# Performance work log

Hardware: AMD Instinct MI355X
Metric: run time of the kernel (lower is better)

## Reference

```python
import jax, jax.numpy as jnp
import numpy as np

N = 2048      # n_nodes
D = 512       # n_channels
AVG_DEG = 16  # average graph degree


def setup_inputs() -> dict:
    key = jax.random.key(0)
    k1, k2, k3 = jax.random.split(key, 3)
    # node features [N, D]
    x = jax.random.normal(k1, (N, D), dtype=jnp.float32)
    # random symmetric graph -> combinatorial Laplacian L = D - A
    E = N * AVG_DEG
    src = jax.random.randint(k2, (E,), 0, N)
    dst = jax.random.randint(k3, (E,), 0, N)
    A = jnp.zeros((N, N), jnp.float32).at[src, dst].add(1.0)
    A = (A + A.T) * 0.5
    A = A * (1.0 - jnp.eye(N, dtype=jnp.float32))  # drop self loops
    deg = A.sum(axis=1)
    L = jnp.diag(deg) - A
    # learned diffusion time (scalar parameter, ic=0.5)
    t = jnp.float32(0.5)
    return {"x": x, "L": L, "t": t}


def reference(x, L, t):
    # forward clamps diffusion_time to >= 1e-8
    tt = jnp.maximum(t, jnp.float32(1e-8))
    # heat kernel: expm(-t * L); the original loops over channels applying
    # compute_diffusion(x[:, [i]], t, L, 'matrix_exp') == expm(-t L) @ x[:, i],
    # which is exactly one dense matmul fused across all channels.
    P = jax.scipy.linalg.expm(-tt * L)  # [N, N]
    return P @ x  # [N, D]
```

## Files before the change

kernel.cpp:

```cpp
#include <hip/hip_runtime.h>

#define N_NODES 2048
#define N_CH    512
#define K_CHEB  48
#define NNZ_MAX 131072
#define NB      256

#define OFF_DIAG   0
#define OFF_SCAL   8192
#define OFF_PERM   12288
#define OFF_BASE   20480
#define OFF_CNTO   28672
#define OFF_GCNT   36864
#define OFF_PKV    40960

__device__ __forceinline__ float b2f(unsigned short u) {
    return __uint_as_float(((unsigned int)u) << 16);
}
__device__ __forceinline__ bool detect32(const unsigned int* tw) {
    return (tw[0] & 0xFFFFu) == 0u;
}
__device__ __forceinline__ unsigned short encE(int col, float v) {
    unsigned int n = (unsigned int)(-2.0f * v + 0.5f);
    return (unsigned short)(((unsigned int)col << 5) | (n & 31u));
}

__global__ void __launch_bounds__(256)
k_prep(const void* __restrict__ Lp, const unsigned int* __restrict__ tw,
       float* __restrict__ diagv, int* __restrict__ basev, int* __restrict__ cnto,
       int* __restrict__ gcnt, unsigned short* __restrict__ pkv) {
    __shared__ unsigned short stage[4][N_NODES];
    __shared__ int scnt[4];
    __shared__ int sbase;
    int w    = threadIdx.x >> 6;
    int lane = threadIdx.x & 63;
    int row  = blockIdx.x * 4 + w;
    bool is32 = detect32(tw);
    int run = 0; float dv = 0.f;
    if (is32) {
        const float4* rf4 = (const float4*)((const float*)Lp + (size_t)row * N_NODES);
        #pragma unroll
        for (int i = 0; i < 8; i++) {
            int j = i * 64 + lane;
            float4 v = rf4[j];
            if (j == (row >> 2)) {
                int rm = row & 3;
                if      (rm == 0) { dv = v.x; v.x = 0.f; }
                else if (rm == 1) { dv = v.y; v.y = 0.f; }
                else if (rm == 2) { dv = v.z; v.z = 0.f; }
                else              { dv = v.w; v.w = 0.f; }
            }
            int c0 = j * 4;
            int lc = (v.x != 0.f) + (v.y != 0.f) + (v.z != 0.f) + (v.w != 0.f);
            int xs = lc;
            #pragma unroll
            for (int d = 1; d < 64; d <<= 1) { int n = __shfl_up(xs, d); if (lane >= d) xs += n; }
            int o = run + xs - lc;
            if (v.x != 0.f) stage[w][o++] = encE(c0 + 0, v.x);
            if (v.y != 0.f) stage[w][o++] = encE(c0 + 1, v.y);
            if (v.z != 0.f) stage[w][o++] = encE(c0 + 2, v.z);
            if (v.w != 0.f) stage[w][o++] = encE(c0 + 3, v.w);
            run += __shfl(xs, 63);
        }
    } else {
        const unsigned short* rp = (const unsigned short*)Lp + (size_t)row * N_NODES;
        for (int c0 = 0; c0 < N_NODES; c0 += 64) {
            float v = b2f(rp[c0 + lane]);
            if (c0 + lane == row) { dv = v; v = 0.f; }
            bool p = (v != 0.f);
            unsigned long long m = __ballot(p);
            int off = __popcll(m & ((1ull << lane) - 1ull));
            if (p) stage[w][run + off] = encE(c0 + lane, v);
            run += (int)__popcll(m);
        }
    }
    #pragma unroll
    for (int o = 32; o; o >>= 1) dv += __shfl_xor(dv, o);
    int padded = (run + 7) & ~7;
    for (int e = run + lane; e < padded; e += 64) stage[w][e] = 0;
    if (lane == 0) scnt[w] = padded;
    __syncthreads();
    if (threadIdx.x == 0)
        sbase = atomicAdd(gcnt, scnt[0] + scnt[1] + scnt[2] + scnt[3]);
    __syncthreads();
    int myb = sbase;
    for (int w2 = 0; w2 < w; w2++) myb += scnt[w2];
    if (lane == 0) { basev[row] = myb; cnto[row] = padded >> 3; diagv[row] = dv; }
    const unsigned int* s32 = (const unsigned int*)stage[w];
    unsigned int* p32 = (unsigned int*)pkv + (myb >> 1);
    for (int i = lane; i < (padded >> 1); i += 64) p32[i] = s32[i];
}

__global__ void k_scan(const float* __restrict__ diagv, float* __restrict__ scal,
                       const void* __restrict__ tp, const int* __restrict__ cnto,
                       int* __restrict__ perm) {
    __shared__ float  fmaxs[256];
    __shared__ double dz[1];
    __shared__ float  cabs[K_CHEB + 1];
    __shared__ int    hist[256];
    __shared__ int    hstart[256];
    int t = threadIdx.x;
    hist[t] = 0;
    float mx = 0.f;
    #pragma unroll
    for (int i = 0; i < 8; i++) mx = fmaxf(mx, diagv[t * 8 + i]);
    fmaxs[t] = mx;
    __syncthreads();
    for (int o = 128; o; o >>= 1) {
        if (t < o) fmaxs[t] = fmaxf(fmaxs[t], fmaxs[t + o]);
        __syncthreads();
    }
    if (t == 0) {
        bool is32 = detect32((const unsigned int*)tp);
        float tt = is32 ? ((const float*)tp)[0] : b2f(((const unsigned short*)tp)[0]);
        tt = fmaxf(tt, 1e-8f);
        float beta = 2.0f * fmaxs[0];
        scal[0] = (beta > 0.f) ? 2.0f / beta : 0.f;
        dz[0] = (beta > 0.f) ? (double)tt * (double)beta * 0.5 : 0.0;
    }
    __syncthreads();
    if (t <= K_CHEB) {
        int k = t;
        double z = dz[0];
        double emz = exp(-z), h = 0.5 * z, h2 = h * h;
        double term = 1.0;
        for (int j = 1; j <= k; j++) term *= h / (double)j;
        double sum = term;
        for (int m = 1; m < 300; m++) {
            term *= h2 / ((double)m * (double)(m + k));
            sum += term;
            if (term == 0.0 || term < sum * 1e-18) break;
        }
        double ck = emz * sum * (k == 0 ? 1.0 : 2.0);
        if (k & 1) ck = -ck;
        scal[16 + k] = (float)ck;
        cabs[k] = (float)fabs(ck);
    }
    __syncthreads();
    if (t == 0) {
        int keff = 1;
        for (int k = K_CHEB; k >= 2; k--)
            if (cabs[k] >= 2.5e-4f) { keff = k; break; }
        scal[1] = (float)keff;
    }
    #pragma unroll
    for (int i = 0; i < 8; i++) {
        int q = min(cnto[t * 8 + i], 255);
        atomicAdd(&hist[q], 1);
    }
    __syncthreads();
    if (t == 0) {
        int acc = 0;
        for (int l = 255; l >= 0; l--) { hstart[l] = acc; acc += hist[l]; }
    }
    __syncthreads();
    #pragma unroll
    for (int i = 0; i < 8; i++) {
        int idx = t * 8 + i;
        int q = min(cnto[idx], 255);
        int pos = atomicAdd(&hstart[q], 1);
        perm[pos] = idx;
    }
}

__device__ __forceinline__ void oct_fma(const float2* __restrict__ cur, uint4 q,
                                        float& ax, float& ay, float& bx, float& by) {
    #pragma unroll
    for (int i = 0; i < 4; i++) {
        unsigned int u = (i == 0) ? q.x : (i == 1) ? q.y : (i == 2) ? q.z : q.w;
        unsigned int e0 = u & 0xFFFFu, e1 = u >> 16;
        float2 c0 = cur[e0 >> 5];
        float2 c1 = cur[e1 >> 5];
        float n0 = (float)(e0 & 31u), n1 = (float)(e1 & 31u);
        ax += n0 * c0.x; ay += n0 * c0.y;
        bx += n1 * c1.x; by += n1 * c1.y;
    }
}

__device__ __forceinline__ float2 gatherO(const float2* __restrict__ cur,
                                          const uint4* __restrict__ s4,
                                          int j0, int j1) {
    float ax = 0.f, ay = 0.f, bx = 0.f, by = 0.f;
    int j = j0;
    if (j + 2 <= j1) {
        uint4 q0 = s4[j], q1 = s4[j + 1];
        j += 2;
        while (j + 2 <= j1) {
            uint4 p0 = s4[j], p1 = s4[j + 1];
            oct_fma(cur, q0, ax, ay, bx, by);
            oct_fma(cur, q1, ax, ay, bx, by);
            q0 = p0; q1 = p1;
            j += 2;
        }
        oct_fma(cur, q0, ax, ay, bx, by);
        oct_fma(cur, q1, ax, ay, bx, by);
    }
    if (j < j1) oct_fma(cur, s4[j], ax, ay, bx, by);
    return make_float2(ax + bx, ay + by);
}

__global__ void __launch_bounds__(1024, 4)
k_cheb(const void* __restrict__ x, const unsigned int* __restrict__ tw,
       const int* __restrict__ basev, const int* __restrict__ cnto,
       const float* __restrict__ diagv, const unsigned short* __restrict__ pkv,
       const float* __restrict__ scal, const int* __restrict__ perm,
       void* __restrict__ out) {
    __shared__ float2 bufA[N_NODES];
    __shared__ float2 bufB[N_NODES];
    __shared__ float  scoef[K_CHEB + 1];
    int t  = threadIdx.x;
    int cb = blockIdx.x * 2;
    bool is32 = detect32(tw);
    if (t <= K_CHEB) scoef[t] = scal[16 + t];
    int ra = perm[t], rb = perm[2047 - t];
    int na = cnto[ra], nb = cnto[rb];
    int pa0 = basev[ra] >> 3, pb0 = basev[rb] >> 3;
    const uint4* s4 = (const uint4*)pkv;
    float da = diagv[ra], db = diagv[rb];
    float g = scal[0];
    int   K = (int)scal[1];

    float2 xa, xb;
    if (is32) {
        xa = *(const float2*)((const float*)x + (size_t)ra * N_CH + cb);
        xb = *(const float2*)((const float*)x + (size_t)rb * N_CH + cb);
    } else {
        const unsigned short* xp = (const unsigned short*)x;
        unsigned int wa = *(const unsigned int*)(xp + (size_t)ra * N_CH + cb);
        unsigned int wb = *(const unsigned int*)(xp + (size_t)rb * N_CH + cb);
        xa = make_float2(b2f((unsigned short)(wa & 0xFFFFu)), b2f((unsigned short)(wa >> 16)));
        xb = make_float2(b2f((unsigned short)(wb & 0xFFFFu)), b2f((unsigned short)(wb >> 16)));
    }
    bufA[ra] = xa; bufA[rb] = xb;
    __syncthreads();

    float gm = -0.5f * g;
    float ia = g * da - 1.f, ib = g * db - 1.f;
    float2 aa = gatherO(bufA, s4, pa0, pa0 + na);
    float2 ab = gatherO(bufA, s4, pb0, pb0 + nb);
    float2 pva = xa, pvb = xb;
    float2 cua = make_float2(gm * aa.x + ia * xa.x, gm * aa.y + ia * xa.y);
    float2 cub = make_float2(gm * ab.x + ib * xb.x, gm * ab.y + ib * xb.y);
    float c0 = scoef[0], c1 = scoef[1];
    float2 oa = make_float2(c0 * xa.x + c1 * cua.x, c0 * xa.y + c1 * cua.y);
    float2 ob = make_float2(c0 * xb.x + c1 * cub.x, c0 * xb.y + c1 * cub.y);
    bufB[ra] = cua; bufB[rb] = cub;
    __syncthreads();

    float gn  = -g;
    float dga = 2.f * g * da - 2.f, dgb = 2.f * g * db - 2.f;
    for (int k = 2; k <= K; k++) {
        const float2* rd = (k & 1) ? bufA : bufB;
        float2*       wr = (k & 1) ? bufB : bufA;
        float ck = scoef[k];
        float2 ba = gatherO(rd, s4, pa0, pa0 + na);
        float2 bb = gatherO(rd, s4, pb0, pb0 + nb);
        float2 tna = make_float2(gn * ba.x + dga * cua.x - pva.x,
                                 gn * ba.y + dga * cua.y - pva.y);
        float2 tnb = make_float2(gn * bb.x + dgb * cub.x - pvb.x,
                                 gn * bb.y + dgb * cub.y - pvb.y);
        pva = cua; cua = tna;
        pvb = cub; cub = tnb;
        oa.x += ck * tna.x; oa.y += ck * tna.y;
        ob.x += ck * tnb.x; ob.y += ck * tnb.y;
        wr[ra] = tna; wr[rb] = tnb;
        __syncthreads();
    }

    if (is32) {
        *(float2*)((float*)out + (size_t)ra * N_CH + cb) = oa;
        *(float2*)((float*)out + (size_t)rb * N_CH + cb) = ob;
    } else {
        unsigned int ua, ub;
        { unsigned int u0 = __float_as_uint(oa.x), u1 = __float_as_uint(oa.y);
          u0 = (u0 + 0x7FFFu + ((u0 >> 16) & 1u)) >> 16;
          u1 = (u1 + 0x7FFFu + ((u1 >> 16) & 1u)) >> 16;
          ua = u0 | (u1 << 16); }
        { unsigned int u0 = __float_as_uint(ob.x), u1 = __float_as_uint(ob.y);
          u0 = (u0 + 0x7FFFu + ((u0 >> 16) & 1u)) >> 16;
          u1 = (u1 + 0x7FFFu + ((u1 >> 16) & 1u)) >> 16;
          ub = u0 | (u1 << 16); }
        *(unsigned int*)((unsigned short*)out + (size_t)ra * N_CH + cb) = ua;
        *(unsigned int*)((unsigned short*)out + (size_t)rb * N_CH + cb) = ub;
    }
}

extern "C" void kernel_launch(void* const* d_in, const int* in_sizes, int n_in,
                              void* d_out, int out_size, void* d_ws, size_t ws_size,
                              hipStream_t stream) {
    const void* x  = d_in[0];
    const void* L  = d_in[1];
    const void* tp = d_in[2];
    const unsigned int* tw = (const unsigned int*)tp;

    char* ws = (char*)d_ws;
    float*          diagv = (float*)          (ws + OFF_DIAG);
    float*          scal  = (float*)          (ws + OFF_SCAL);
    int*            perm  = (int*)            (ws + OFF_PERM);
    int*            basev = (int*)            (ws + OFF_BASE);
    int*            cnto  = (int*)            (ws + OFF_CNTO);
    int*            gcnt  = (int*)            (ws + OFF_GCNT);
    unsigned short* pkv   = (unsigned short*) (ws + OFF_PKV);

    hipMemsetAsync(gcnt, 0, 4, stream);
    k_prep<<<512, 256, 0, stream>>>(L, tw, diagv, basev, cnto, gcnt, pkv);
    k_scan<<<1,   256, 0, stream>>>(diagv, scal, tp, cnto, perm);
    k_cheb<<<NB, 1024, 0, stream>>>(x, tw, basev, cnto, diagv, pkv, scal, perm, d_out);
}
```

Measured before the change: 177.4 us.

## Use fixed-capacity sparse rows and bank-rotate entries to cut LDS conflicts

Each row's packed sparse entries now sit in a fixed 128-slot region instead of a space handed out by a global atomic. This removes the memset, the atomic offset allocation and the base-offset array. A new k_bank kernel reorders each row's entries by column bank group, rotated by the row's thread slot, so lanes of a wavefront gather from the shared-memory vector on different LDS banks at the same step. In exchange there is an extra kernel launch, and rows with more than 128 nonzeros would be truncated, which is only enforced on the bf16 path.

```diff
diff --git a/kernel.cpp b/kernel.cpp
--- a/kernel.cpp
+++ b/kernel.cpp
@@ -3,16 +3,16 @@
 #define N_NODES 2048
 #define N_CH    512
 #define K_CHEB  48
-#define NNZ_MAX 131072
+#define ROW_CAP 128
 #define NB      256
 
 #define OFF_DIAG   0
 #define OFF_SCAL   8192
 #define OFF_PERM   12288
-#define OFF_BASE   20480
+#define OFF_ROT    20480
 #define OFF_CNTO   28672
-#define OFF_GCNT   36864
 #define OFF_PKV    40960
+#define OFF_PKV2   (40960 + 524288)
 
 __device__ __forceinline__ float b2f(unsigned short u) {
     return __uint_as_float(((unsigned int)u) << 16);
@@ -27,11 +27,9 @@
 
 __global__ void __launch_bounds__(256)
 k_prep(const void* __restrict__ Lp, const unsigned int* __restrict__ tw,
-       float* __restrict__ diagv, int* __restrict__ basev, int* __restrict__ cnto,
-       int* __restrict__ gcnt, unsigned short* __restrict__ pkv) {
+       float* __restrict__ diagv, int* __restrict__ cnto,
+       unsigned short* __restrict__ pkv) {
     __shared__ unsigned short stage[4][N_NODES];
-    __shared__ int scnt[4];
-    __shared__ int sbase;
     int w    = threadIdx.x >> 6;
     int lane = threadIdx.x & 63;
     int row  = blockIdx.x * 4 + w;
@@ -70,30 +68,24 @@
             bool p = (v != 0.f);
             unsigned long long m = __ballot(p);
             int off = __popcll(m & ((1ull << lane) - 1ull));
-            if (p) stage[w][run + off] = encE(c0 + lane, v);
+            if (p && run + off < ROW_CAP) stage[w][run + off] = encE(c0 + lane, v);
             run += (int)__popcll(m);
         }
     }
     #pragma unroll
     for (int o = 32; o; o >>= 1) dv += __shfl_xor(dv, o);
+    run = min(run, ROW_CAP);
     int padded = (run + 7) & ~7;
     for (int e = run + lane; e < padded; e += 64) stage[w][e] = 0;
-    if (lane == 0) scnt[w] = padded;
-    __syncthreads();
-    if (threadIdx.x == 0)
-        sbase = atomicAdd(gcnt, scnt[0] + scnt[1] + scnt[2] + scnt[3]);
-    __syncthreads();
-    int myb = sbase;
-    for (int w2 = 0; w2 < w; w2++) myb += scnt[w2];
-    if (lane == 0) { basev[row] = myb; cnto[row] = padded >> 3; diagv[row] = dv; }
+    if (lane == 0) { cnto[row] = padded >> 3; diagv[row] = dv; }
     const unsigned int* s32 = (const unsigned int*)stage[w];
-    unsigned int* p32 = (unsigned int*)pkv + (myb >> 1);
+    unsigned int* p32 = (unsigned int*)pkv + row * (ROW_CAP / 2);
     for (int i = lane; i < (padded >> 1); i += 64) p32[i] = s32[i];
 }
 
 __global__ void k_scan(const float* __restrict__ diagv, float* __restrict__ scal,
                        const void* __restrict__ tp, const int* __restrict__ cnto,
-                       int* __restrict__ perm) {
+                       int* __restrict__ perm, int* __restrict__ rot16) {
     __shared__ float  fmaxs[256];
     __shared__ double dz[1];
     __shared__ float  cabs[K_CHEB + 1];
@@ -160,6 +152,35 @@
         int q = min(cnto[idx], 255);
         int pos = atomicAdd(&hstart[q], 1);
         perm[pos] = idx;
+        int thr = (pos < 1024) ? pos : (2047 - pos);
+        rot16[idx] = thr & 15;
+    }
+}
+
+__global__ void __launch_bounds__(256)
+k_bank(const unsigned short* __restrict__ pkv, const int* __restrict__ cnto,
+       const int* __restrict__ rot16, unsigned short* __restrict__ pkv2) {
+    int wid  = (blockIdx.x * blockDim.x + threadIdx.x) >> 6;
+    int lane = threadIdx.x & 63;
+    if (wid >= N_NODES) return;
+    int n   = cnto[wid] * 8;
+    int rot = rot16[wid];
+    const unsigned short* src = pkv  + wid * ROW_CAP;
+    unsigned short*       dst = pkv2 + wid * ROW_CAP;
+    bool v0 = lane < n, v1 = lane + 64 < n;
+    unsigned short e0 = v0 ? src[lane]      : 0;
+    unsigned short e1 = v1 ? src[lane + 64] : 0;
+    int k0 = ((int)((e0 >> 5) & 15) - rot) & 15;
+    int k1 = ((int)((e1 >> 5) & 15) - rot) & 15;
+    int pos = 0;
+    #pragma unroll
+    for (int b = 0; b < 16; b++) {
+        unsigned long long m0 = __ballot(v0 && k0 == b);
+        unsigned long long m1 = __ballot(v1 && k1 == b);
+        int c0 = __popcll(m0);
+        if (v0 && k0 == b) dst[pos +      __popcll(m0 & ((1ull << lane) - 1ull))] = e0;
+        if (v1 && k1 == b) dst[pos + c0 + __popcll(m1 & ((1ull << lane) - 1ull))] = e1;
+        pos += c0 + __popcll(m1);
     }
 }
 
@@ -201,10 +222,9 @@
 
 __global__ void __launch_bounds__(1024, 4)
 k_cheb(const void* __restrict__ x, const unsigned int* __restrict__ tw,
-       const int* __restrict__ basev, const int* __restrict__ cnto,
-       const float* __restrict__ diagv, const unsigned short* __restrict__ pkv,
-       const float* __restrict__ scal, const int* __restrict__ perm,
-       void* __restrict__ out) {
+       const int* __restrict__ cnto, const float* __restrict__ diagv,
+       const unsigned short* __restrict__ pkv2, const float* __restrict__ scal,
+       const int* __restrict__ perm, void* __restrict__ out) {
     __shared__ float2 bufA[N_NODES];
     __shared__ float2 bufB[N_NODES];
     __shared__ float  scoef[K_CHEB + 1];
@@ -214,8 +234,8 @@
     if (t <= K_CHEB) scoef[t] = scal[16 + t];
     int ra = perm[t], rb = perm[2047 - t];
     int na = cnto[ra], nb = cnto[rb];
-    int pa0 = basev[ra] >> 3, pb0 = basev[rb] >> 3;
-    const uint4* s4 = (const uint4*)pkv;
+    int pa0 = ra * (ROW_CAP / 8), pb0 = rb * (ROW_CAP / 8);
+    const uint4* s4 = (const uint4*)pkv2;
     float da = diagv[ra], db = diagv[rb];
     float g = scal[0];
     int   K = (int)scal[1];
@@ -297,13 +317,13 @@
     float*          diagv = (float*)          (ws + OFF_DIAG);
     float*          scal  = (float*)          (ws + OFF_SCAL);
     int*            perm  = (int*)            (ws + OFF_PERM);
-    int*            basev = (int*)            (ws + OFF_BASE);
+    int*            rot16 = (int*)            (ws + OFF_ROT);
     int*            cnto  = (int*)            (ws + OFF_CNTO);
-    int*            gcnt  = (int*)            (ws + OFF_GCNT);
     unsigned short* pkv   = (unsigned short*) (ws + OFF_PKV);
-
-    hipMemsetAsync(gcnt, 0, 4, stream);
-    k_prep<<<512, 256, 0, stream>>>(L, tw, diagv, basev, cnto, gcnt, pkv);
-    k_scan<<<1,   256, 0, stream>>>(diagv, scal, tp, cnto, perm);
-    k_cheb<<<NB, 1024, 0, stream>>>(x, tw, basev, cnto, diagv, pkv, scal, perm, d_out);
-}
+    unsigned short* pkv2  = (unsigned short*) (ws + OFF_PKV2);
+
+    k_prep<<<512, 256, 0, stream>>>(L, tw, diagv, cnto, pkv);
+    k_scan<<<1,   256, 0, stream>>>(diagv, scal, tp, cnto, perm, rot16);
+    k_bank<<<512, 256, 0, stream>>>(pkv, cnto, rot16, pkv2);
+    k_cheb<<<NB, 1024, 0, stream>>>(x, tw, cnto, diagv, pkv2, scal, perm, d_out);
+}
```

Measured after the change: 178.6 us. About the same (+0.7%).

## Tighten spectral bound with edge-based estimate and raise Chebyshev truncation threshold

Applied to the files above, without the earlier changes.

Adds a kernel that computes a tighter upper bound on the Laplacian's largest eigenvalue as the max over edges of d_i + d_j, replacing the 2*max-degree bound. A smaller spectral interval lowers z and so the number of Chebyshev terms needed. The coefficient cutoff for choosing the effective degree is also raised, which truncates the series earlier. Both cut the number of sparse matvec iterations, at the cost of an extra kernel launch and a looser accuracy margin.

```diff
diff --git a/kernel.cpp b/kernel.cpp
--- a/kernel.cpp
+++ b/kernel.cpp
@@ -91,30 +91,39 @@
     for (int i = lane; i < (padded >> 1); i += 64) p32[i] = s32[i];
 }
 
-__global__ void k_scan(const float* __restrict__ diagv, float* __restrict__ scal,
-                       const void* __restrict__ tp, const int* __restrict__ cnto,
+__global__ void __launch_bounds__(256)
+k_edge(const float* __restrict__ diagv, const int* __restrict__ basev,
+       const int* __restrict__ cnto, const unsigned short* __restrict__ pkv,
+       int* __restrict__ betam) {
+    int wid  = (blockIdx.x * blockDim.x + threadIdx.x) >> 6;
+    int lane = threadIdx.x & 63;
+    if (wid >= N_NODES) return;
+    float dr = diagv[wid];
+    int b = basev[wid], ne = cnto[wid] * 8;
+    float mx = 0.f;
+    for (int e = lane; e < ne; e += 64) {
+        unsigned short u = pkv[b + e];
+        if (u & 31u) mx = fmaxf(mx, dr + diagv[u >> 5]);
+    }
+    #pragma unroll
+    for (int o = 32; o; o >>= 1) mx = fmaxf(mx, __shfl_xor(mx, o));
+    if (lane == 0) atomicMax(betam, __float_as_int(mx));
+}
+
+__global__ void k_scan(float* __restrict__ scal, const void* __restrict__ tp,
+                       const int* __restrict__ cnto, const int* __restrict__ betam,
                        int* __restrict__ perm) {
-    __shared__ float  fmaxs[256];
     __shared__ double dz[1];
     __shared__ float  cabs[K_CHEB + 1];
     __shared__ int    hist[256];
     __shared__ int    hstart[256];
     int t = threadIdx.x;
     hist[t] = 0;
-    float mx = 0.f;
-    #pragma unroll
-    for (int i = 0; i < 8; i++) mx = fmaxf(mx, diagv[t * 8 + i]);
-    fmaxs[t] = mx;
-    __syncthreads();
-    for (int o = 128; o; o >>= 1) {
-        if (t < o) fmaxs[t] = fmaxf(fmaxs[t], fmaxs[t + o]);
-        __syncthreads();
-    }
     if (t == 0) {
         bool is32 = detect32((const unsigned int*)tp);
         float tt = is32 ? ((const float*)tp)[0] : b2f(((const unsigned short*)tp)[0]);
         tt = fmaxf(tt, 1e-8f);
-        float beta = 2.0f * fmaxs[0];
+        float beta = __int_as_float(betam[0]);
         scal[0] = (beta > 0.f) ? 2.0f / beta : 0.f;
         dz[0] = (beta > 0.f) ? (double)tt * (double)beta * 0.5 : 0.0;
     }
@@ -140,7 +149,7 @@
     if (t == 0) {
         int keff = 1;
         for (int k = K_CHEB; k >= 2; k--)
-            if (cabs[k] >= 2.5e-4f) { keff = k; break; }
+            if (cabs[k] >= 4e-4f) { keff = k; break; }
         scal[1] = (float)keff;
     }
     #pragma unroll
@@ -302,8 +311,9 @@
     int*            gcnt  = (int*)            (ws + OFF_GCNT);
     unsigned short* pkv   = (unsigned short*) (ws + OFF_PKV);
 
-    hipMemsetAsync(gcnt, 0, 4, stream);
+    hipMemsetAsync(gcnt, 0, 8, stream);
     k_prep<<<512, 256, 0, stream>>>(L, tw, diagv, basev, cnto, gcnt, pkv);
-    k_scan<<<1,   256, 0, stream>>>(diagv, scal, tp, cnto, perm);
+    k_edge<<<512, 256, 0, stream>>>(diagv, basev, cnto, pkv, gcnt + 1);
+    k_scan<<<1,   256, 0, stream>>>(scal, tp, cnto, gcnt + 1, perm);
     k_cheb<<<NB, 1024, 0, stream>>>(x, tw, basev, cnto, diagv, pkv, scal, perm, d_out);
 }
```

Measured after the change: 196.9 us. 11.0% more time.

## Fold scan kernel into Chebyshev kernel and use fixed-capacity per-row sparse storage

Applied to the files above, without the earlier changes.

Removes the memset and the single-block k_scan launch. Each k_cheb block now redundantly computes the spectral bound, the Chebyshev coefficients, the row permutation histogram and the effective degree in shared memory. Rows are stored at a fixed 96-entry capacity, which drops the global atomic offset allocation, but any row with more nonzeros is silently truncated. The spectral bound becomes the maximum of d_i + d_j over edges, which is tighter than 2*max(d), and the coefficient cutoff is loosened from 2.5e-4 to 4e-4, so fewer Chebyshev terms may run at some cost in accuracy.

```diff
diff --git a/kernel.cpp b/kernel.cpp
--- a/kernel.cpp
+++ b/kernel.cpp
@@ -3,16 +3,13 @@
 #define N_NODES 2048
 #define N_CH    512
 #define K_CHEB  48
-#define NNZ_MAX 131072
+#define ROW_CAP 96
+#define ROW_OCT (ROW_CAP / 8)
 #define NB      256
 
 #define OFF_DIAG   0
-#define OFF_SCAL   8192
-#define OFF_PERM   12288
-#define OFF_BASE   20480
-#define OFF_CNTO   28672
-#define OFF_GCNT   36864
-#define OFF_PKV    40960
+#define OFF_CNTO   8192
+#define OFF_PKV    16384
 
 __device__ __forceinline__ float b2f(unsigned short u) {
     return __uint_as_float(((unsigned int)u) << 16);
@@ -27,11 +24,9 @@
 
 __global__ void __launch_bounds__(256)
 k_prep(const void* __restrict__ Lp, const unsigned int* __restrict__ tw,
-       float* __restrict__ diagv, int* __restrict__ basev, int* __restrict__ cnto,
-       int* __restrict__ gcnt, unsigned short* __restrict__ pkv) {
+       float* __restrict__ diagv, int* __restrict__ cnto,
+       unsigned short* __restrict__ pkv) {
     __shared__ unsigned short stage[4][N_NODES];
-    __shared__ int scnt[4];
-    __shared__ int sbase;
     int w    = threadIdx.x >> 6;
     int lane = threadIdx.x & 63;
     int row  = blockIdx.x * 4 + w;
@@ -76,91 +71,13 @@
     }
     #pragma unroll
     for (int o = 32; o; o >>= 1) dv += __shfl_xor(dv, o);
+    run = min(run, ROW_CAP);
     int padded = (run + 7) & ~7;
     for (int e = run + lane; e < padded; e += 64) stage[w][e] = 0;
-    if (lane == 0) scnt[w] = padded;
-    __syncthreads();
-    if (threadIdx.x == 0)
-        sbase = atomicAdd(gcnt, scnt[0] + scnt[1] + scnt[2] + scnt[3]);
-    __syncthreads();
-    int myb = sbase;
-    for (int w2 = 0; w2 < w; w2++) myb += scnt[w2];
-    if (lane == 0) { basev[row] = myb; cnto[row] = padded >> 3; diagv[row] = dv; }
+    if (lane == 0) { cnto[row] = padded >> 3; diagv[row] = dv; }
     const unsigned int* s32 = (const unsigned int*)stage[w];
-    unsigned int* p32 = (unsigned int*)pkv + (myb >> 1);
+    unsigned int* p32 = (unsigned int*)pkv + row * (ROW_CAP / 2);
     for (int i = lane; i < (padded >> 1); i += 64) p32[i] = s32[i];
-}
-
-__global__ void k_scan(const float* __restrict__ diagv, float* __restrict__ scal,
-                       const void* __restrict__ tp, const int* __restrict__ cnto,
-                       int* __restrict__ perm) {
-    __shared__ float  fmaxs[256];
-    __shared__ double dz[1];
-    __shared__ float  cabs[K_CHEB + 1];
-    __shared__ int    hist[256];
-    __shared__ int    hstart[256];
-    int t = threadIdx.x;
-    hist[t] = 0;
-    float mx = 0.f;
-    #pragma unroll
-    for (int i = 0; i < 8; i++) mx = fmaxf(mx, diagv[t * 8 + i]);
-    fmaxs[t] = mx;
-    __syncthreads();
-    for (int o = 128; o; o >>= 1) {
-        if (t < o) fmaxs[t] = fmaxf(fmaxs[t], fmaxs[t + o]);
-        __syncthreads();
-    }
-    if (t == 0) {
-        bool is32 = detect32((const unsigned int*)tp);
-        float tt = is32 ? ((const float*)tp)[0] : b2f(((const unsigned short*)tp)[0]);
-        tt = fmaxf(tt, 1e-8f);
-        float beta = 2.0f * fmaxs[0];
-        scal[0] = (beta > 0.f) ? 2.0f / beta : 0.f;
-        dz[0] = (beta > 0.f) ? (double)tt * (double)beta * 0.5 : 0.0;
-    }
-    __syncthreads();
-    if (t <= K_CHEB) {
-        int k = t;
-        double z = dz[0];
-        double emz = exp(-z), h = 0.5 * z, h2 = h * h;
-        double term = 1.0;
-        for (int j = 1; j <= k; j++) term *= h / (double)j;
-        double sum = term;
-        for (int m = 1; m < 300; m++) {
-            term *= h2 / ((double)m * (double)(m + k));
-            sum += term;
-            if (term == 0.0 || term < sum * 1e-18) break;
-        }
-        double ck = emz * sum * (k == 0 ? 1.0 : 2.0);
-        if (k & 1) ck = -ck;
-        scal[16 + k] = (float)ck;
-        cabs[k] = (float)fabs(ck);
-    }
-    __syncthreads();
-    if (t == 0) {
-        int keff = 1;
-        for (int k = K_CHEB; k >= 2; k--)
-            if (cabs[k] >= 2.5e-4f) { keff = k; break; }
-        scal[1] = (float)keff;
-    }
-    #pragma unroll
-    for (int i = 0; i < 8; i++) {
-        int q = min(cnto[t * 8 + i], 255);
-        atomicAdd(&hist[q], 1);
-    }
-    __syncthreads();
-    if (t == 0) {
-        int acc = 0;
-        for (int l = 255; l >= 0; l--) { hstart[l] = acc; acc += hist[l]; }
-    }
-    __syncthreads();
-    #pragma unroll
-    for (int i = 0; i < 8; i++) {
-        int idx = t * 8 + i;
-        int q = min(cnto[idx], 255);
-        int pos = atomicAdd(&hstart[q], 1);
-        perm[pos] = idx;
-    }
 }
 
 __device__ __forceinline__ void oct_fma(const float2* __restrict__ cur, uint4 q,
@@ -201,24 +118,110 @@
 
 __global__ void __launch_bounds__(1024, 4)
 k_cheb(const void* __restrict__ x, const unsigned int* __restrict__ tw,
-       const int* __restrict__ basev, const int* __restrict__ cnto,
-       const float* __restrict__ diagv, const unsigned short* __restrict__ pkv,
-       const float* __restrict__ scal, const int* __restrict__ perm,
-       void* __restrict__ out) {
-    __shared__ float2 bufA[N_NODES];
-    __shared__ float2 bufB[N_NODES];
+       const int* __restrict__ cnto, const float* __restrict__ diagv,
+       const unsigned short* __restrict__ pkv, void* __restrict__ out) {
+    __shared__ float  bufA2[N_NODES * 2];
+    __shared__ float  bufB2[N_NODES * 2];
+    __shared__ float  sdiag[N_NODES];
+    __shared__ int    sperm[N_NODES];
+    __shared__ int    scnt[N_NODES];
     __shared__ float  scoef[K_CHEB + 1];
+    __shared__ float  cabs[K_CHEB + 1];
+    __shared__ int    hist[256];
+    __shared__ int    ibeta;
+    __shared__ double dzs;
+    __shared__ int    skeff;
+    float2* bufA = (float2*)bufA2;
+    float2* bufB = (float2*)bufB2;
+
     int t  = threadIdx.x;
     int cb = blockIdx.x * 2;
     bool is32 = detect32(tw);
-    if (t <= K_CHEB) scoef[t] = scal[16 + t];
-    int ra = perm[t], rb = perm[2047 - t];
-    int na = cnto[ra], nb = cnto[rb];
-    int pa0 = basev[ra] >> 3, pb0 = basev[rb] >> 3;
+    int r0 = t, r1 = t + 1024;
+
+    sdiag[r0] = diagv[r0]; sdiag[r1] = diagv[r1];
+    int q0 = cnto[r0], q1 = cnto[r1];
+    scnt[r0] = q0; scnt[r1] = q1;
+    if (t < 256) hist[t] = 0;
+    if (t == 0) ibeta = 0;
+    __syncthreads();
+    {
+        const uint4* s4 = (const uint4*)pkv;
+        float mx = 0.f;
+        #pragma unroll
+        for (int rr = 0; rr < 2; rr++) {
+            int r  = rr ? r1 : r0;
+            int no = rr ? q1 : q0;
+            float dr = sdiag[r];
+            for (int j = 0; j < no; j++) {
+                uint4 q = s4[r * ROW_OCT + j];
+                #pragma unroll
+                for (int i = 0; i < 4; i++) {
+                    unsigned int u = (i == 0) ? q.x : (i == 1) ? q.y : (i == 2) ? q.z : q.w;
+                    unsigned int e0 = u & 0xFFFFu, e1 = u >> 16;
+                    if (e0 & 31u) mx = fmaxf(mx, dr + sdiag[e0 >> 5]);
+                    if (e1 & 31u) mx = fmaxf(mx, dr + sdiag[e1 >> 5]);
+                }
+            }
+        }
+        atomicMax(&ibeta, __float_as_int(mx));
+        atomicAdd(&hist[q0], 1);
+        atomicAdd(&hist[q1], 1);
+    }
+    __syncthreads();
+    if (t == 0) {
+        float tt = is32 ? ((const float*)tw)[0] : b2f((unsigned short)(tw[0] & 0xFFFFu));
+        tt = fmaxf(tt, 1e-8f);
+        float beta = __int_as_float(ibeta);
+        dzs = (beta > 0.f) ? (double)tt * (double)beta * 0.5 : 0.0;
+        scoef[0] = 0.f;
+        int acc = 0;
+        for (int l = 255; l >= 0; l--) { int c = hist[l]; hist[l] = acc; acc += c; }
+    }
+    __syncthreads();
+    if (t <= K_CHEB) {
+        int k = t;
+        double z = dzs;
+        double emz = exp(-z), h = 0.5 * z, h2 = h * h;
+        double term = 1.0;
+        for (int j = 1; j <= k; j++) term *= h / (double)j;
+        double sum = term;
+        for (int m = 1; m < 300; m++) {
+            term *= h2 / ((double)m * (double)(m + k));
+            sum += term;
+            if (term == 0.0 || term < sum * 1e-18) break;
+        }
+        double ck = emz * sum * (k == 0 ? 1.0 : 2.0);
+        if (k & 1) ck = -ck;
+        scoef[k] = (float)ck;
+        cabs[k] = (float)fabs(ck);
+    }
+    {
+        int p0 = atomicAdd(&hist[q0], 1); sperm[p0] = r0;
+        int p1 = atomicAdd(&hist[q1], 1); sperm[p1] = r1;
+    }
+    __syncthreads();
+    if (t == 0) {
+        int keff = 1;
+        for (int k = K_CHEB; k >= 2; k--)
+            if (cabs[k] >= 4e-4f) { keff = k; break; }
+        skeff = keff;
+    }
+    __syncthreads();
+
+    int ra = sperm[t], rb = sperm[2047 - t];
+    int na = scnt[ra], nb = scnt[rb];
+    int pa0 = ra * ROW_OCT, pb0 = rb * ROW_OCT;
     const uint4* s4 = (const uint4*)pkv;
-    float da = diagv[ra], db = diagv[rb];
-    float g = scal[0];
-    int   K = (int)scal[1];
+    float da = sdiag[ra], db = sdiag[rb];
+    double zb = dzs;
+    float g = (zb > 0.0) ? (float)(1.0 / (zb / fmax((double)(is32 ? ((const float*)tw)[0]
+                        : b2f((unsigned short)(tw[0] & 0xFFFFu))), 1e-8))) : 0.f;
+    {
+        float beta = __int_as_float(ibeta);
+        g = (beta > 0.f) ? 2.0f / beta : 0.f;
+    }
+    int K = skeff;
 
     float2 xa, xb;
     if (is32) {
@@ -295,15 +298,9 @@
 
     char* ws = (char*)d_ws;
     float*          diagv = (float*)          (ws + OFF_DIAG);
-    float*          scal  = (float*)          (ws + OFF_SCAL);
-    int*            perm  = (int*)            (ws + OFF_PERM);
-    int*            basev = (int*)            (ws + OFF_BASE);
     int*            cnto  = (int*)            (ws + OFF_CNTO);
-    int*            gcnt  = (int*)            (ws + OFF_GCNT);
     unsigned short* pkv   = (unsigned short*) (ws + OFF_PKV);
 
-    hipMemsetAsync(gcnt, 0, 4, stream);
-    k_prep<<<512, 256, 0, stream>>>(L, tw, diagv, basev, cnto, gcnt, pkv);
-    k_scan<<<1,   256, 0, stream>>>(diagv, scal, tp, cnto, perm);
-    k_cheb<<<NB, 1024, 0, stream>>>(x, tw, basev, cnto, diagv, pkv, scal, perm, d_out);
-}
+    k_prep<<<512, 256, 0, stream>>>(L, tw, diagv, cnto, pkv);
+    k_cheb<<<NB, 1024, 0, stream>>>(x, tw, cnto, diagv, pkv, d_out);
+}
```

New measurement: 186.3 us. 1.05x slower.
